# Kernel optimization log

Hardware: AMD Instinct MI355X
Metric: run time of the kernel (lower is better)

Reference implementation:

```python
import jax, jax.numpy as jnp
import numpy as np

B, H, P, L = 16, 128, 64, 8192  # batch, d_input, d_state, seq_len
TWO_PI = 6.283185307179586


def setup_inputs() -> dict:
    key = jax.random.key(0)
    k_u, k_lr, k_li, k_br, k_bi, k_cr, k_ci, k_d = jax.random.split(key, 8)
    u = jax.random.normal(k_u, (B, H, L), dtype=jnp.float32)
    # continuous-time diagonal state matrix: Lambda = -rand + i*2*pi*rand
    lam_re = -jax.random.uniform(k_lr, (P,), dtype=jnp.float32)
    lam_im = TWO_PI * jax.random.uniform(k_li, (P,), dtype=jnp.float32)
    Lam = lam_re + 1j * lam_im                       # (P,) complex64
    Lambda_bar = jnp.exp(Lam)                        # ZOH with Delta=1
    # continuous B, then ZOH: B_bar = (Lambda_bar - 1)/Lambda * B
    Bc = (jax.random.normal(k_br, (P, H), dtype=jnp.float32)
          + 1j * jax.random.normal(k_bi, (P, H), dtype=jnp.float32))
    B_bar = ((Lambda_bar - 1.0) / Lam)[:, None] * Bc  # (P,H) complex64
    C = (jax.random.normal(k_cr, (H, P), dtype=jnp.float32)
         + 1j * jax.random.normal(k_ci, (H, P), dtype=jnp.float32))
    D = jax.random.normal(k_d, (H, H), dtype=jnp.float32)
    return {
        "u": u,
        "Lambda_re": jnp.real(Lambda_bar).astype(jnp.float32),
        "Lambda_im": jnp.imag(Lambda_bar).astype(jnp.float32),
        "B_re": jnp.real(B_bar).astype(jnp.float32),
        "B_im": jnp.imag(B_bar).astype(jnp.float32),
        "C_re": jnp.real(C).astype(jnp.float32),
        "C_im": jnp.imag(C).astype(jnp.float32),
        "D": D,
    }


def _binary_op(elem_i, elem_j):
    # diagonal linear recurrence combine: (A^i, Bu_i) o (A^j, Bu_j)
    a_i, bu_i = elem_i
    a_j, bu_j = elem_j
    return a_j * a_i, a_j * bu_i + bu_j


def reference(u, Lambda_re, Lambda_im, B_re, B_im, C_re, C_im, D):
    Lambda_bar = Lambda_re + 1j * Lambda_im           # (P,)
    B_bar = B_re + 1j * B_im                          # (P,H)
    C = C_re + 1j * C_im                              # (H,P)
    uc = u.astype(B_bar.dtype)                        # (B,H,L) complex
    Bu = jnp.einsum('ph,bhl->bpl', B_bar, uc)         # (B,P,L)
    A = jnp.broadcast_to(Lambda_bar[None, :, None], Bu.shape)
    # parallel associative scan of the diagonal linear recurrence over L
    _, xs = jax.lax.associative_scan(_binary_op, (A, Bu), axis=2)  # (B,P,L)
    C_A_Bu = jnp.einsum('hp,bpl->bhl', C, xs).real    # (B,H,L)
    # einsum('hh,bhl->bhl', D, u) uses only the diagonal of D
    Du = jnp.diagonal(D)[None, :, None] * u           # (B,H,L)
    return jax.nn.gelu(C_A_Bu + Du, approximate=False)
```

## Files before the change

kernel.cpp:

```cpp
#include <hip/hip_runtime.h>
#include <math.h>

#define NB 16
#define NH 128
#define NP 64
#define NL 8192
#define NCHUNK 64

__global__ __launch_bounds__(256) void k_bu_scan(
    const float* __restrict__ u, const float* __restrict__ Bre,
    const float* __restrict__ Bim, const float* __restrict__ Lre,
    const float* __restrict__ Lim, float2* __restrict__ xloc,
    float2* __restrict__ Echunk) {
  __shared__ __align__(16) float sBre[32][68];
  __shared__ float sBim[32][68];
  __shared__ float sU[32][128];
  const int b  = blockIdx.y;
  const int c  = blockIdx.x;
  const int l0 = c * 128;
  const int t  = threadIdx.x;
  const int tp = t & 15;
  const int tl = t >> 4;
  float accRe[4][8], accIm[4][8];
  #pragma unroll
  for (int i = 0; i < 4; ++i)
    #pragma unroll
    for (int j = 0; j < 8; ++j) { accRe[i][j] = 0.f; accIm[i][j] = 0.f; }

  for (int ht = 0; ht < 4; ++ht) {
    const int h0 = ht * 32;
    #pragma unroll
    for (int idx = t; idx < 2048; idx += 256) {
      int h = idx & 31, p = idx >> 5;
      sBre[h][p] = Bre[p * NH + h0 + h];
      sBim[h][p] = Bim[p * NH + h0 + h];
    }
    #pragma unroll
    for (int idx = t; idx < 32 * 128; idx += 256) {
      int l = idx & 127, h = idx >> 7;
      sU[h][l] = u[((size_t)(b * NH + h0 + h)) * NL + l0 + l];
    }
    __syncthreads();
    #pragma unroll 4
    for (int h = 0; h < 32; ++h) {
      float4 br4 = *(const float4*)&sBre[h][tp * 4];
      float4 bi4 = *(const float4*)&sBim[h][tp * 4];
      float4 ua  = *(const float4*)&sU[h][tl * 8];
      float4 ub  = *(const float4*)&sU[h][tl * 8 + 4];
      float uu[8] = {ua.x, ua.y, ua.z, ua.w, ub.x, ub.y, ub.z, ub.w};
      float brr[4] = {br4.x, br4.y, br4.z, br4.w};
      float bii[4] = {bi4.x, bi4.y, bi4.z, bi4.w};
      #pragma unroll
      for (int i = 0; i < 4; ++i)
        #pragma unroll
        for (int j = 0; j < 8; ++j) {
          accRe[i][j] = fmaf(brr[i], uu[j], accRe[i][j]);
          accIm[i][j] = fmaf(bii[i], uu[j], accIm[i][j]);
        }
    }
    __syncthreads();
  }

  float lr[4], li[4];
  #pragma unroll
  for (int i = 0; i < 4; ++i) { lr[i] = Lre[tp * 4 + i]; li[i] = Lim[tp * 4 + i]; }
  #pragma unroll
  for (int i = 0; i < 4; ++i) {
    float xr = 0.f, xi = 0.f;
    #pragma unroll
    for (int j = 0; j < 8; ++j) {
      float nr = fmaf(lr[i], xr, fmaf(-li[i], xi, accRe[i][j]));
      float ni = fmaf(lr[i], xi, fmaf( li[i], xr, accIm[i][j]));
      xr = nr; xi = ni; accRe[i][j] = xr; accIm[i][j] = xi;
    }
  }

  float2* E = reinterpret_cast<float2*>(&sBre[0][0]);
  #define EL(p, q) E[(p) * 17 + (q)]
  #pragma unroll
  for (int i = 0; i < 4; ++i)
    EL(tp * 4 + i, tl) = make_float2(accRe[i][7], accIm[i][7]);

  float wr[4], wi[4];
  #pragma unroll
  for (int i = 0; i < 4; ++i) {
    float ar = lr[i], ai = li[i];
    #pragma unroll
    for (int k = 0; k < 3; ++k) { float nr = ar * ar - ai * ai; ai = 2.f * ar * ai; ar = nr; }
    wr[i] = ar; wi[i] = ai;
  }
  __syncthreads();
  #pragma unroll
  for (int d = 1; d < 16; d <<= 1) {
    float2 rv[4];
    #pragma unroll
    for (int i = 0; i < 4; ++i)
      rv[i] = (tl >= d) ? EL(tp * 4 + i, tl - d) : make_float2(0.f, 0.f);
    __syncthreads();
    if (tl >= d) {
      #pragma unroll
      for (int i = 0; i < 4; ++i) {
        float2 cur = EL(tp * 4 + i, tl);
        cur.x += wr[i] * rv[i].x - wi[i] * rv[i].y;
        cur.y += wr[i] * rv[i].y + wi[i] * rv[i].x;
        EL(tp * 4 + i, tl) = cur;
      }
    }
    __syncthreads();
    #pragma unroll
    for (int i = 0; i < 4; ++i) {
      float nr = wr[i] * wr[i] - wi[i] * wi[i];
      wi[i] = 2.f * wr[i] * wi[i]; wr[i] = nr;
    }
  }

  float2 cin[4];
  #pragma unroll
  for (int i = 0; i < 4; ++i)
    cin[i] = (tl > 0) ? EL(tp * 4 + i, tl - 1) : make_float2(0.f, 0.f);
  if (t < 64) {
    float2 tot = EL(t, 15);
    Echunk[((size_t)(b * NCHUNK + c)) * NP + t] = tot;
  }

  #pragma unroll
  for (int i = 0; i < 4; ++i) {
    float cr = cin[i].x, ci = cin[i].y;
    #pragma unroll
    for (int j = 0; j < 8; ++j) {
      float nr = lr[i] * cr - li[i] * ci;
      float nc = lr[i] * ci + li[i] * cr;
      cr = nr; ci = nc;
      accRe[i][j] += cr; accIm[i][j] += ci;
    }
  }

  #pragma unroll
  for (int i = 0; i < 4; ++i) {
    size_t base = ((size_t)(b * NP + tp * 4 + i)) * NL + l0 + tl * 8;
    #pragma unroll
    for (int j = 0; j < 8; j += 2) {
      float4 v = make_float4(accRe[i][j], accIm[i][j], accRe[i][j + 1], accIm[i][j + 1]);
      *(float4*)&xloc[base + j] = v;
    }
  }
  #undef EL
}

__global__ void k_carry(const float2* __restrict__ Echunk,
                        const float* __restrict__ Lre, const float* __restrict__ Lim,
                        float2* __restrict__ carryg, float2* __restrict__ powtab) {
  const int b = blockIdx.x, p = threadIdx.x;
  const float lr = Lre[p], li = Lim[p];
  float wr = lr, wi = li;
  #pragma unroll
  for (int k = 0; k < 7; ++k) { float nr = wr * wr - wi * wi; wi = 2.f * wr * wi; wr = nr; }
  float xr = 0.f, xi = 0.f;
  for (int c = 0; c < NCHUNK; ++c) {
    carryg[((size_t)(b * NCHUNK + c)) * NP + p] = make_float2(xr, xi);
    float2 e = Echunk[((size_t)(b * NCHUNK + c)) * NP + p];
    float nr = e.x + wr * xr - wi * xi;
    float ni = e.y + wr * xi + wi * xr;
    xr = nr; xi = ni;
  }
  if (b == 0) {
    float pr = 1.f, pi = 0.f;
    for (int j = 0; j < 128; ++j) {
      float nr = pr * lr - pi * li;
      pi = pr * li + pi * lr; pr = nr;
      powtab[p * 128 + j] = make_float2(pr, pi);
    }
  }
}

__global__ __launch_bounds__(256) void k_out(
    const float2* __restrict__ xs, const float* __restrict__ u,
    const float* __restrict__ Cre, const float* __restrict__ Cim,
    const float* __restrict__ D, const float2* __restrict__ carryg,
    const float2* __restrict__ powtab, float* __restrict__ out) {
  __shared__ float sCre[16][132];
  __shared__ float sCim[16][132];
  __shared__ float sXre[16][128];
  __shared__ float sXim[16][128];
  __shared__ float sDd[128];
  const int b  = blockIdx.y;
  const int c  = blockIdx.x;
  const int l0 = c * 128;
  const int t  = threadIdx.x;
  const int lane = t & 63, w = t >> 6;
  const int th = (lane & 7) + 8 * (w & 1);
  const int tl = (lane >> 3) + 8 * (w >> 1);
  const int lfix = t & 127;
  const int ppb  = t >> 7;

  if (t < 128) sDd[t] = D[t * NH + t];

  float acc[8][8];
  #pragma unroll
  for (int i = 0; i < 8; ++i)
    #pragma unroll
    for (int j = 0; j < 8; ++j) acc[i][j] = 0.f;

  float2 gx[8], gp[8], gc[8];
  #pragma unroll
  for (int k = 0; k < 8; ++k) {
    int pp = ppb + 2 * k;
    gx[k] = xs[((size_t)(b * NP + pp)) * NL + l0 + lfix];
    gp[k] = powtab[pp * 128 + lfix];
    gc[k] = carryg[((size_t)(b * NCHUNK + c)) * NP + pp];
  }

  #pragma unroll
  for (int pt = 0; pt < 4; ++pt) {
    const int p0 = pt * 16;
    __syncthreads();
    #pragma unroll
    for (int idx = t; idx < 2048; idx += 256) {
      int pp = idx & 15, h = idx >> 4;
      sCre[pp][h] = Cre[h * NP + p0 + pp];
      sCim[pp][h] = Cim[h * NP + p0 + pp];
    }
    #pragma unroll
    for (int k = 0; k < 8; ++k) {
      int pp = ppb + 2 * k;
      float xr = gx[k].x + gp[k].x * gc[k].x - gp[k].y * gc[k].y;
      float xi = gx[k].y + gp[k].x * gc[k].y + gp[k].y * gc[k].x;
      sXre[pp][lfix] = xr; sXim[pp][lfix] = xi;
    }
    __syncthreads();
    if (pt < 3) {
      const int p1 = (pt + 1) * 16;
      #pragma unroll
      for (int k = 0; k < 8; ++k) {
        int pp = ppb + 2 * k;
        gx[k] = xs[((size_t)(b * NP + p1 + pp)) * NL + l0 + lfix];
        gp[k] = powtab[(p1 + pp) * 128 + lfix];
        gc[k] = carryg[((size_t)(b * NCHUNK + c)) * NP + p1 + pp];
      }
    }
    #pragma unroll 4
    for (int pp = 0; pp < 16; ++pp) {
      float4 ca = *(const float4*)&sCre[pp][th * 8];
      float4 cb = *(const float4*)&sCre[pp][th * 8 + 4];
      float4 ia = *(const float4*)&sCim[pp][th * 8];
      float4 ib = *(const float4*)&sCim[pp][th * 8 + 4];
      float4 xa = *(const float4*)&sXre[pp][tl * 8];
      float4 xb = *(const float4*)&sXre[pp][tl * 8 + 4];
      float4 ya = *(const float4*)&sXim[pp][tl * 8];
      float4 yb = *(const float4*)&sXim[pp][tl * 8 + 4];
      float cr[8] = {ca.x, ca.y, ca.z, ca.w, cb.x, cb.y, cb.z, cb.w};
      float ci[8] = {ia.x, ia.y, ia.z, ia.w, ib.x, ib.y, ib.z, ib.w};
      float xr[8] = {xa.x, xa.y, xa.z, xa.w, xb.x, xb.y, xb.z, xb.w};
      float xi[8] = {ya.x, ya.y, ya.z, ya.w, yb.x, yb.y, yb.z, yb.w};
      #pragma unroll
      for (int i = 0; i < 8; ++i)
        #pragma unroll
        for (int j = 0; j < 8; ++j) {
          acc[i][j] = fmaf(cr[i], xr[j], acc[i][j]);
          acc[i][j] = fmaf(-ci[i], xi[j], acc[i][j]);
        }
    }
  }

  #pragma unroll
  for (int i = 0; i < 8; ++i) {
    const int h = th * 8 + i;
    const float dd = sDd[h];
    size_t rb = ((size_t)(b * NH + h)) * NL + l0 + tl * 8;
    float4 u0 = *(const float4*)&u[rb];
    float4 u1 = *(const float4*)&u[rb + 4];
    float uu[8] = {u0.x, u0.y, u0.z, u0.w, u1.x, u1.y, u1.z, u1.w};
    float r[8];
    #pragma unroll
    for (int j = 0; j < 8; ++j) {
      float vv = acc[i][j] + dd * uu[j];
      r[j] = 0.5f * vv * (1.0f + erff(vv * 0.70710678118654752f));
    }
    *(float4*)&out[rb]     = make_float4(r[0], r[1], r[2], r[3]);
    *(float4*)&out[rb + 4] = make_float4(r[4], r[5], r[6], r[7]);
  }
}

extern "C" void kernel_launch(void* const* d_in, const int* in_sizes, int n_in,
                              void* d_out, int out_size, void* d_ws, size_t ws_size,
                              hipStream_t stream) {
  (void)in_sizes; (void)n_in; (void)out_size; (void)ws_size;
  const float* u   = (const float*)d_in[0];
  const float* Lre = (const float*)d_in[1];
  const float* Lim = (const float*)d_in[2];
  const float* Bre = (const float*)d_in[3];
  const float* Bim = (const float*)d_in[4];
  const float* Cre = (const float*)d_in[5];
  const float* Cim = (const float*)d_in[6];
  const float* Dm  = (const float*)d_in[7];
  float* out = (float*)d_out;

  char* wsb = (char*)d_ws;
  float2* xloc   = (float2*)wsb;
  float2* Echunk = (float2*)(wsb + 67108864);
  float2* carryg = (float2*)(wsb + 67108864 + 524288);
  float2* powtab = (float2*)(wsb + 67108864 + 1048576);

  dim3 g(NL / 128, NB);
  k_bu_scan<<<g, 256, 0, stream>>>(u, Bre, Bim, Lre, Lim, xloc, Echunk);
  k_carry<<<NB, NP, 0, stream>>>(Echunk, Lre, Lim, carryg, powtab);
  k_out<<<g, 256, 0, stream>>>(xloc, u, Cre, Cim, Dm, carryg, powtab, out);
}
```

Baseline: 264.0 us.

## Store local scan states as packed bf16 and parallelize carry scan across chunks

The intermediate local scan states are rounded to bf16 and packed as re/im pairs into one 32-bit word. This halves the workspace traffic written by the first kernel and read by the output kernel. The carry kernel now runs one wavefront per (batch, state) and does a Hillis-Steele shuffle scan over the 64 chunks. It also computes the power table by exponentiation by squaring instead of a serial loop. The cost is lower precision in the intermediate states, which may hurt accuracy.

```diff
diff --git a/kernel.cpp b/kernel.cpp
--- a/kernel.cpp
+++ b/kernel.cpp
@@ -7,10 +7,14 @@
 #define NL 8192
 #define NCHUNK 64
 
+__device__ __forceinline__ unsigned toBF(unsigned u) {
+  return (u + 0x7FFFu + ((u >> 16) & 1u)) >> 16;
+}
+
 __global__ __launch_bounds__(256) void k_bu_scan(
     const float* __restrict__ u, const float* __restrict__ Bre,
     const float* __restrict__ Bim, const float* __restrict__ Lre,
-    const float* __restrict__ Lim, float2* __restrict__ xloc,
+    const float* __restrict__ Lim, unsigned* __restrict__ xbf,
     float2* __restrict__ Echunk) {
   __shared__ __align__(16) float sBre[32][68];
   __shared__ float sBim[32][68];
@@ -138,43 +142,66 @@
   #pragma unroll
   for (int i = 0; i < 4; ++i) {
     size_t base = ((size_t)(b * NP + tp * 4 + i)) * NL + l0 + tl * 8;
-    #pragma unroll
-    for (int j = 0; j < 8; j += 2) {
-      float4 v = make_float4(accRe[i][j], accIm[i][j], accRe[i][j + 1], accIm[i][j + 1]);
-      *(float4*)&xloc[base + j] = v;
-    }
+    uint4 w0, w1;
+    w0.x = toBF(__float_as_uint(accRe[i][0])) | (toBF(__float_as_uint(accIm[i][0])) << 16);
+    w0.y = toBF(__float_as_uint(accRe[i][1])) | (toBF(__float_as_uint(accIm[i][1])) << 16);
+    w0.z = toBF(__float_as_uint(accRe[i][2])) | (toBF(__float_as_uint(accIm[i][2])) << 16);
+    w0.w = toBF(__float_as_uint(accRe[i][3])) | (toBF(__float_as_uint(accIm[i][3])) << 16);
+    w1.x = toBF(__float_as_uint(accRe[i][4])) | (toBF(__float_as_uint(accIm[i][4])) << 16);
+    w1.y = toBF(__float_as_uint(accRe[i][5])) | (toBF(__float_as_uint(accIm[i][5])) << 16);
+    w1.z = toBF(__float_as_uint(accRe[i][6])) | (toBF(__float_as_uint(accIm[i][6])) << 16);
+    w1.w = toBF(__float_as_uint(accRe[i][7])) | (toBF(__float_as_uint(accIm[i][7])) << 16);
+    *(uint4*)&xbf[base]     = w0;
+    *(uint4*)&xbf[base + 4] = w1;
   }
   #undef EL
 }
 
-__global__ void k_carry(const float2* __restrict__ Echunk,
-                        const float* __restrict__ Lre, const float* __restrict__ Lim,
-                        float2* __restrict__ carryg, float2* __restrict__ powtab) {
-  const int b = blockIdx.x, p = threadIdx.x;
+__global__ __launch_bounds__(64) void k_carry(
+    const float2* __restrict__ Echunk, const float* __restrict__ Lre,
+    const float* __restrict__ Lim, float2* __restrict__ carryg,
+    float2* __restrict__ powtab) {
+  const int p = blockIdx.x;
+  const int b = blockIdx.y;
+  const int t = threadIdx.x;
   const float lr = Lre[p], li = Lim[p];
   float wr = lr, wi = li;
   #pragma unroll
   for (int k = 0; k < 7; ++k) { float nr = wr * wr - wi * wi; wi = 2.f * wr * wi; wr = nr; }
-  float xr = 0.f, xi = 0.f;
-  for (int c = 0; c < NCHUNK; ++c) {
-    carryg[((size_t)(b * NCHUNK + c)) * NP + p] = make_float2(xr, xi);
-    float2 e = Echunk[((size_t)(b * NCHUNK + c)) * NP + p];
-    float nr = e.x + wr * xr - wi * xi;
-    float ni = e.y + wr * xi + wi * xr;
-    xr = nr; xi = ni;
-  }
+  float2 e = Echunk[((size_t)(b * NCHUNK + t)) * NP + p];
+  float sr = e.x, si = e.y;
+  float fr = wr, fi = wi;
+  #pragma unroll
+  for (int d = 1; d < 64; d <<= 1) {
+    float pr = __shfl_up(sr, d);
+    float pi = __shfl_up(si, d);
+    if (t >= d) { sr += fr * pr - fi * pi; si += fr * pi + fi * pr; }
+    float nr = fr * fr - fi * fi; fi = 2.f * fr * fi; fr = nr;
+  }
+  float cr = __shfl_up(sr, 1);
+  float ci = __shfl_up(si, 1);
+  if (t == 0) { cr = 0.f; ci = 0.f; }
+  carryg[((size_t)(b * NCHUNK + t)) * NP + p] = make_float2(cr, ci);
+
   if (b == 0) {
-    float pr = 1.f, pi = 0.f;
-    for (int j = 0; j < 128; ++j) {
-      float nr = pr * lr - pi * li;
-      pi = pr * li + pi * lr; pr = nr;
-      powtab[p * 128 + j] = make_float2(pr, pi);
-    }
+    float ar = lr, ai = li, br = 1.f, bi = 0.f;
+    int e1 = t + 1;
+    while (e1) {
+      if (e1 & 1) { float nr = br * ar - bi * ai; bi = br * ai + bi * ar; br = nr; }
+      float nr = ar * ar - ai * ai; ai = 2.f * ar * ai; ar = nr;
+      e1 >>= 1;
+    }
+    powtab[p * 128 + t] = make_float2(br, bi);
+    float qr = lr, qi = li;
+    #pragma unroll
+    for (int k = 0; k < 6; ++k) { float nr = qr * qr - qi * qi; qi = 2.f * qr * qi; qr = nr; }
+    float hr = br * qr - bi * qi, hi = br * qi + bi * qr;
+    powtab[p * 128 + t + 64] = make_float2(hr, hi);
   }
 }
 
 __global__ __launch_bounds__(256) void k_out(
-    const float2* __restrict__ xs, const float* __restrict__ u,
+    const unsigned* __restrict__ xs, const float* __restrict__ u,
     const float* __restrict__ Cre, const float* __restrict__ Cim,
     const float* __restrict__ D, const float2* __restrict__ carryg,
     const float2* __restrict__ powtab, float* __restrict__ out) {
@@ -201,11 +228,11 @@
     #pragma unroll
     for (int j = 0; j < 8; ++j) acc[i][j] = 0.f;
 
-  float2 gx[8], gp[8], gc[8];
+  unsigned xg[8]; float2 gp[8], gc[8];
   #pragma unroll
   for (int k = 0; k < 8; ++k) {
     int pp = ppb + 2 * k;
-    gx[k] = xs[((size_t)(b * NP + pp)) * NL + l0 + lfix];
+    xg[k] = xs[((size_t)(b * NP + pp)) * NL + l0 + lfix];
     gp[k] = powtab[pp * 128 + lfix];
     gc[k] = carryg[((size_t)(b * NCHUNK + c)) * NP + pp];
   }
@@ -223,8 +250,10 @@
     #pragma unroll
     for (int k = 0; k < 8; ++k) {
       int pp = ppb + 2 * k;
-      float xr = gx[k].x + gp[k].x * gc[k].x - gp[k].y * gc[k].y;
-      float xi = gx[k].y + gp[k].x * gc[k].y + gp[k].y * gc[k].x;
+      float xlr = __uint_as_float(xg[k] << 16);
+      float xli = __uint_as_float(xg[k] & 0xFFFF0000u);
+      float xr = xlr + gp[k].x * gc[k].x - gp[k].y * gc[k].y;
+      float xi = xli + gp[k].x * gc[k].y + gp[k].y * gc[k].x;
       sXre[pp][lfix] = xr; sXim[pp][lfix] = xi;
     }
     __syncthreads();
@@ -233,7 +262,7 @@
       #pragma unroll
       for (int k = 0; k < 8; ++k) {
         int pp = ppb + 2 * k;
-        gx[k] = xs[((size_t)(b * NP + p1 + pp)) * NL + l0 + lfix];
+        xg[k] = xs[((size_t)(b * NP + p1 + pp)) * NL + l0 + lfix];
         gp[k] = powtab[(p1 + pp) * 128 + lfix];
         gc[k] = carryg[((size_t)(b * NCHUNK + c)) * NP + p1 + pp];
       }
@@ -296,13 +325,14 @@
   float* out = (float*)d_out;
 
   char* wsb = (char*)d_ws;
-  float2* xloc   = (float2*)wsb;
-  float2* Echunk = (float2*)(wsb + 67108864);
-  float2* carryg = (float2*)(wsb + 67108864 + 524288);
-  float2* powtab = (float2*)(wsb + 67108864 + 1048576);
+  unsigned* xbf  = (unsigned*)wsb;
+  float2* Echunk = (float2*)(wsb + 33554432);
+  float2* carryg = (float2*)(wsb + 33554432 + 524288);
+  float2* powtab = (float2*)(wsb + 33554432 + 1048576);
 
   dim3 g(NL / 128, NB);
-  k_bu_scan<<<g, 256, 0, stream>>>(u, Bre, Bim, Lre, Lim, xloc, Echunk);
-  k_carry<<<NB, NP, 0, stream>>>(Echunk, Lre, Lim, carryg, powtab);
-  k_out<<<g, 256, 0, stream>>>(xloc, u, Cre, Cim, Dm, carryg, powtab, out);
-}
+  k_bu_scan<<<g, 256, 0, stream>>>(u, Bre, Bim, Lre, Lim, xbf, Echunk);
+  dim3 gc(NP, NB);
+  k_carry<<<gc, 64, 0, stream>>>(Echunk, Lre, Lim, carryg, powtab);
+  k_out<<<g, 256, 0, stream>>>(xbf, u, Cre, Cim, Dm, carryg, powtab, out);
+}
```

New measurement: 292.8 us. +10.9%, slower.
